# Kernel optimization log

Hardware: AMD Instinct MI355X
Metric: run time of the kernel (lower is better)

Reference implementation:

```python
import jax, jax.numpy as jnp
import numpy as np
import math

D_MODEL = 4096
N_HEADS = 32
D_HEAD = D_MODEL // N_HEADS
SEQ = 2048
BATCH = 1


def rope(x):
    # x: [B, H, S, D]; rotate pairs (even, odd) along last dim
    S = x.shape[2]
    D = x.shape[-1]
    theta = 1.0 / (10000.0 ** (jnp.arange(0, D, 2, dtype=jnp.float32) / D))  # [D/2]
    ang = jnp.arange(S, dtype=jnp.float32)[:, None] * theta[None, :]          # [S, D/2]
    cos = jnp.cos(ang)
    sin = jnp.sin(ang)
    x_even = x[..., ::2]
    x_odd = x[..., 1::2]
    rot_even = x_even * cos - x_odd * sin
    rot_odd = x_even * sin + x_odd * cos
    return jnp.stack((rot_even, rot_odd), axis=-1).reshape(x.shape)


def setup_inputs() -> dict:
    key = jax.random.key(0)
    ks = jax.random.split(key, 9)
    scale = 1.0 / math.sqrt(D_MODEL)
    return {
        "x": jax.random.normal(ks[0], (BATCH, SEQ, D_MODEL), dtype=jnp.float32),
        "Wq": jax.random.normal(ks[1], (D_MODEL, D_MODEL), dtype=jnp.float32) * scale,
        "bq": jnp.zeros((D_MODEL,), dtype=jnp.float32),
        "Wk": jax.random.normal(ks[2], (D_MODEL, D_MODEL), dtype=jnp.float32) * scale,
        "bk": jnp.zeros((D_MODEL,), dtype=jnp.float32),
        "Wv": jax.random.normal(ks[3], (D_MODEL, D_MODEL), dtype=jnp.float32) * scale,
        "bv": jnp.zeros((D_MODEL,), dtype=jnp.float32),
        "Wo": jax.random.normal(ks[4], (D_MODEL, D_MODEL), dtype=jnp.float32) * scale,
        "bo": jnp.zeros((D_MODEL,), dtype=jnp.float32),
    }


def reference(x, Wq, bq, Wk, bk, Wv, bv, Wo, bo):
    B, S, _ = x.shape
    def proj(W, b):
        h = x @ W.T + b  # torch Linear convention: y = x W^T + b
        return h.reshape(B, S, N_HEADS, D_HEAD).transpose(0, 2, 1, 3)  # [B,H,S,D]
    Q = rope(proj(Wq, bq))
    K = rope(proj(Wk, bk))
    V = proj(Wv, bv)
    scores = jnp.einsum('bhqd,bhkd->bhqk', Q, K) / math.sqrt(D_HEAD)
    causal = jnp.tril(jnp.ones((S, S), dtype=bool))
    scores = jnp.where(causal[None, None], scores, jnp.float32(-jnp.inf))
    attn = jax.nn.softmax(scores, axis=-1)
    out = jnp.einsum('bhqk,bhkd->bhqd', attn, V)
    out = out.transpose(0, 2, 1, 3).reshape(B, S, N_HEADS * D_HEAD)
    return out @ Wo.T + bo
```

## Files before the change

kernel.cpp:

```cpp
#include <hip/hip_runtime.h>
#include <hip/hip_bf16.h>

typedef __bf16 bf16x8 __attribute__((ext_vector_type(8)));
typedef float floatx4 __attribute__((ext_vector_type(4)));

__device__ __forceinline__ ushort f2bf(float f) {
  union { float f; unsigned u; } v; v.f = f;
  unsigned r = ((v.u >> 16) & 1u) + 0x7FFFu;
  return (ushort)((v.u + r) >> 16);
}
__device__ __forceinline__ float bf2f(ushort u) {
  union { unsigned u; float f; } v; v.u = ((unsigned)u) << 16;
  return v.f;
}

__device__ __forceinline__ void cp16(const void* g, void* l) {
  __builtin_amdgcn_global_load_lds((const __attribute__((address_space(1))) unsigned int*)g,
                                   (__attribute__((address_space(3))) unsigned int*)l,
                                   16, 0, 0);
}

__global__ __launch_bounds__(256) void cast_kernel(const float* __restrict__ in,
                                                   ushort* __restrict__ out) {
  size_t idx = (size_t)blockIdx.x * 256 + threadIdx.x;
  float4 v = ((const float4*)in)[idx];
  ushort4 o;
  o.x = f2bf(v.x); o.y = f2bf(v.y); o.z = f2bf(v.z); o.w = f2bf(v.w);
  ((ushort4*)out)[idx] = o;
}

template <int EPI>
__global__ __launch_bounds__(256) void gemm_bt(const ushort* __restrict__ A,
                                               const ushort* __restrict__ B,
                                               const float* __restrict__ bias,
                                               void* __restrict__ outp) {
  constexpr int K = 4096, N = 4096;
  __shared__ ushort As[2][128 * 32];
  __shared__ ushort Bs[2][128 * 32];

  unsigned bid = blockIdx.x;
  unsigned swz = (bid & 7u) * (gridDim.x >> 3) + (bid >> 3);
  int tm = swz >> 5;
  int tn = swz & 31;
  int m0 = tm << 7, n0 = tn << 7;

  int t = threadIdx.x;
  int l = t & 63;
  int w = t >> 6;
  int wm = (w >> 1) << 6;
  int wn = (w & 1) << 6;

  floatx4 zero4 = {0.f, 0.f, 0.f, 0.f};
  floatx4 acc[4][4];
#pragma unroll
  for (int i = 0; i < 4; ++i)
#pragma unroll
    for (int j = 0; j < 4; ++j) acc[i][j] = zero4;

  int rr = t >> 2;
  int sp = t & 3;

  auto stage = [&](int buf, int kt) {
    int k0 = kt << 5;
#pragma unroll
    for (int iss = 0; iss < 2; ++iss) {
      int r = iss * 64 + rr;
      int sl = sp ^ (r & 3);
      cp16(A + (size_t)(m0 + r) * K + k0 + sl * 8, &As[buf][(iss * 256 + t) * 8]);
      cp16(B + (size_t)(n0 + r) * K + k0 + sl * 8, &Bs[buf][(iss * 256 + t) * 8]);
    }
  };

  stage(0, 0);
  __syncthreads();
  int buf = 0;
  for (int kt = 0; kt < K / 32; ++kt) {
    if (kt + 1 < K / 32) stage(buf ^ 1, kt + 1);
    bf16x8 af[4], bfr[4];
#pragma unroll
    for (int i = 0; i < 4; ++i) {
      int ra = wm + i * 16 + (l & 15);
      af[i] = *(const bf16x8*)&As[buf][ra * 32 + (((l >> 4) ^ (ra & 3)) * 8)];
      int rb = wn + i * 16 + (l & 15);
      bfr[i] = *(const bf16x8*)&Bs[buf][rb * 32 + (((l >> 4) ^ (rb & 3)) * 8)];
    }
#pragma unroll
    for (int i = 0; i < 4; ++i)
#pragma unroll
      for (int j = 0; j < 4; ++j)
        acc[i][j] = __builtin_amdgcn_mfma_f32_16x16x32_bf16(af[i], bfr[j], acc[i][j], 0, 0, 0);
    __syncthreads();
    buf ^= 1;
  }

#pragma unroll
  for (int i = 0; i < 4; ++i)
#pragma unroll
    for (int j = 0; j < 4; ++j)
#pragma unroll
      for (int r = 0; r < 4; ++r) {
        int row = m0 + wm + i * 16 + ((l >> 4) << 2) + r;
        int col = n0 + wn + j * 16 + (l & 15);
        float v = acc[i][j][r] + bias[col];
        if constexpr (EPI == 0) {
          ((ushort*)outp)[((size_t)(col >> 7) * 2048 + row) * 128 + (col & 127)] = f2bf(v);
        } else {
          ((float*)outp)[(size_t)row * N + col] = v;
        }
      }
}

__global__ __launch_bounds__(256) void rope_kernel(ushort* __restrict__ Q,
                                                   ushort* __restrict__ K) {
  unsigned idx = blockIdx.x * 256 + threadIdx.x;
  ushort* p = blockIdx.y ? K : Q;
  int i4 = idx & 15;
  int s = (idx >> 4) & 2047;
  size_t base = ((size_t)(idx >> 15) * 2048 + s) * 128 + (size_t)i4 * 8;
  ushort v[8];
  *(uint4*)v = *(const uint4*)(p + base);
  const float C = 0.14391156516f;
#pragma unroll
  for (int j = 0; j < 4; ++j) {
    int i = i4 * 4 + j;
    float theta = expf(-C * (float)i);
    float ang = (float)s * theta;
    float cs = cosf(ang), sn = sinf(ang);
    float e = bf2f(v[2 * j]), o = bf2f(v[2 * j + 1]);
    v[2 * j]     = f2bf(e * cs - o * sn);
    v[2 * j + 1] = f2bf(e * sn + o * cs);
  }
  *(uint4*)(p + base) = *(uint4*)v;
}

__global__ __launch_bounds__(256) void transpose_v(const ushort* __restrict__ V,
                                                   ushort* __restrict__ Vt) {
  __shared__ ushort tile[64][72];
  int st = blockIdx.x, dt = blockIdx.y, h = blockIdx.z;
  int t = threadIdx.x;
  int rl = t >> 2, c16 = (t & 3) * 16;
  const ushort* src = V + ((size_t)(h * 2048 + st * 64 + rl)) * 128 + dt * 64 + c16;
  *(uint4*)&tile[rl][c16] = *(const uint4*)src;
  *(uint4*)&tile[rl][c16 + 8] = *(const uint4*)(src + 8);
  __syncthreads();
  int d = t >> 2, s16 = (t & 3) * 16;
  __align__(16) ushort tmp[16];
#pragma unroll
  for (int j = 0; j < 16; ++j) tmp[j] = tile[s16 + j][d];
  ushort* dst = Vt + ((size_t)(h * 128 + dt * 64 + d)) * 2048 + st * 64 + s16;
  *(uint4*)dst = *(uint4*)tmp;
  *(uint4*)(dst + 8) = *(uint4*)(tmp + 8);
}

__global__ __launch_bounds__(256) void attn_kernel(const ushort* __restrict__ Qb,
                                                   const ushort* __restrict__ Kb,
                                                   const ushort* __restrict__ Vt,
                                                   ushort* __restrict__ aO) {
  __shared__ ushort Ks[64 * 128];
  __shared__ ushort Vs[128 * 64];
  __shared__ ushort Ps[4][16 * 64];

  int qt = blockIdx.x;
  int h = blockIdx.y;
  int t = threadIdx.x;
  int l = t & 63;
  int w = t >> 6;

  bf16x8 qf[4];
  {
    int qrow = qt * 64 + w * 16 + (l & 15);
    const ushort* qp = Qb + ((size_t)(h * 2048 + qrow)) * 128 + ((l >> 4) * 8);
#pragma unroll
    for (int ks = 0; ks < 4; ++ks) qf[ks] = *(const bf16x8*)(qp + ks * 32);
  }

  float m[4], lsum[4];
#pragma unroll
  for (int r = 0; r < 4; ++r) { m[r] = -1e30f; lsum[r] = 0.f; }
  floatx4 zero4 = {0.f, 0.f, 0.f, 0.f};
  floatx4 oacc[8];
#pragma unroll
  for (int i = 0; i < 8; ++i) oacc[i] = zero4;

  const float scale = 0.08838834764831845f;

  for (int kt = 0; kt <= qt; ++kt) {
    {
      int rk = t >> 4, sk = t & 15;
      int rv = t >> 3, sv = t & 7;
#pragma unroll
      for (int iss = 0; iss < 4; ++iss) {
        int row = iss * 16 + rk;
        int sl = sk ^ (row & 7);
        cp16(Kb + ((size_t)(h * 2048 + kt * 64 + row)) * 128 + sl * 8,
             &Ks[(iss * 256 + t) * 8]);
        int rowv = iss * 32 + rv;
        int slv = sv ^ (rowv & 7);
        cp16(Vt + ((size_t)(h * 128 + rowv)) * 2048 + kt * 64 + slv * 8,
             &Vs[(iss * 256 + t) * 8]);
      }
    }
    __syncthreads();

    floatx4 sacc[4];
#pragma unroll
    for (int nt = 0; nt < 4; ++nt) sacc[nt] = zero4;
#pragma unroll
    for (int nt = 0; nt < 4; ++nt) {
      int row = nt * 16 + (l & 15);
#pragma unroll
      for (int ks = 0; ks < 4; ++ks) {
        bf16x8 kf = *(const bf16x8*)&Ks[row * 128 + (((ks * 4 + (l >> 4)) ^ (row & 7)) * 8)];
        sacc[nt] = __builtin_amdgcn_mfma_f32_16x16x32_bf16(qf[ks], kf, sacc[nt], 0, 0, 0);
      }
    }

    float sv_[4][4];
    float mt[4] = {-1e30f, -1e30f, -1e30f, -1e30f};
#pragma unroll
    for (int nt = 0; nt < 4; ++nt)
#pragma unroll
      for (int r = 0; r < 4; ++r) {
        float s = sacc[nt][r] * scale;
        if (kt == qt) {
          int kg = nt * 16 + (l & 15);
          int qg = w * 16 + ((l >> 4) << 2) + r;
          if (kg > qg) s = -1e30f;
        }
        sv_[nt][r] = s;
        mt[r] = fmaxf(mt[r], s);
      }
#pragma unroll
    for (int r = 0; r < 4; ++r)
#pragma unroll
      for (int msk = 1; msk < 16; msk <<= 1) mt[r] = fmaxf(mt[r], __shfl_xor(mt[r], msk, 64));

    float sf[4], mn[4];
#pragma unroll
    for (int r = 0; r < 4; ++r) {
      mn[r] = fmaxf(m[r], mt[r]);
      sf[r] = __expf(m[r] - mn[r]);
      m[r] = mn[r];
    }
#pragma unroll
    for (int i = 0; i < 8; ++i)
#pragma unroll
      for (int r = 0; r < 4; ++r) oacc[i][r] *= sf[r];

    float ps[4] = {0.f, 0.f, 0.f, 0.f};
    ushort* Pw = Ps[w];
#pragma unroll
    for (int nt = 0; nt < 4; ++nt)
#pragma unroll
      for (int r = 0; r < 4; ++r) {
        float p = __expf(sv_[nt][r] - mn[r]);
        ps[r] += p;
        int row = ((l >> 4) << 2) + r;
        int col = nt * 16 + (l & 15);
        int slot = (col >> 3) ^ (row & 7);
        Pw[row * 64 + slot * 8 + (col & 7)] = f2bf(p);
      }
#pragma unroll
    for (int r = 0; r < 4; ++r) {
#pragma unroll
      for (int msk = 1; msk < 16; msk <<= 1) ps[r] += __shfl_xor(ps[r], msk, 64);
      lsum[r] = lsum[r] * sf[r] + ps[r];
    }

    bf16x8 pf[2];
#pragma unroll
    for (int ks = 0; ks < 2; ++ks) {
      int row = l & 15;
      pf[ks] = *(const bf16x8*)&Pw[row * 64 + (((ks * 4 + (l >> 4)) ^ (row & 7)) * 8)];
    }
#pragma unroll
    for (int nt = 0; nt < 8; ++nt) {
      int row = nt * 16 + (l & 15);
#pragma unroll
      for (int ks = 0; ks < 2; ++ks) {
        bf16x8 vf = *(const bf16x8*)&Vs[row * 64 + (((ks * 4 + (l >> 4)) ^ (row & 7)) * 8)];
        oacc[nt] = __builtin_amdgcn_mfma_f32_16x16x32_bf16(pf[ks], vf, oacc[nt], 0, 0, 0);
      }
    }
    __syncthreads();
  }

  float inv[4];
#pragma unroll
  for (int r = 0; r < 4; ++r) inv[r] = 1.0f / lsum[r];
#pragma unroll
  for (int nt = 0; nt < 8; ++nt)
#pragma unroll
    for (int r = 0; r < 4; ++r) {
      int row = qt * 64 + w * 16 + ((l >> 4) << 2) + r;
      int col = h * 128 + nt * 16 + (l & 15);
      aO[(size_t)row * 4096 + col] = f2bf(oacc[nt][r] * inv[r]);
    }
}

extern "C" void kernel_launch(void* const* d_in, const int* in_sizes, int n_in,
                              void* d_out, int out_size, void* d_ws, size_t ws_size,
                              hipStream_t stream) {
  const float* x  = (const float*)d_in[0];
  const float* Wq = (const float*)d_in[1];
  const float* bq = (const float*)d_in[2];
  const float* Wk = (const float*)d_in[3];
  const float* bk = (const float*)d_in[4];
  const float* Wv = (const float*)d_in[5];
  const float* bv = (const float*)d_in[6];
  const float* Wo = (const float*)d_in[7];
  const float* bo = (const float*)d_in[8];
  float* out = (float*)d_out;

  char* ws = (char*)d_ws;
  ushort* Wb = (ushort*)(ws);
  ushort* xb = (ushort*)(ws + 33554432);
  ushort* Qb = (ushort*)(ws + 50331648);
  ushort* Kb = (ushort*)(ws + 67108864);
  ushort* Vb = (ushort*)(ws + 83886080);
  ushort* Vt = xb;
  ushort* aO = Vb;

  cast_kernel<<<8192, 256, 0, stream>>>(x, xb);
  cast_kernel<<<16384, 256, 0, stream>>>(Wq, Wb);
  gemm_bt<0><<<512, 256, 0, stream>>>(xb, Wb, bq, Qb);
  cast_kernel<<<16384, 256, 0, stream>>>(Wk, Wb);
  gemm_bt<0><<<512, 256, 0, stream>>>(xb, Wb, bk, Kb);
  cast_kernel<<<16384, 256, 0, stream>>>(Wv, Wb);
  gemm_bt<0><<<512, 256, 0, stream>>>(xb, Wb, bv, Vb);
  rope_kernel<<<dim3(4096, 2), 256, 0, stream>>>(Qb, Kb);
  transpose_v<<<dim3(32, 2, 32), 256, 0, stream>>>(Vb, Vt);
  attn_kernel<<<dim3(32, 32), 256, 0, stream>>>(Qb, Kb, Vt, aO);
  cast_kernel<<<16384, 256, 0, stream>>>(Wo, Wb);
  gemm_bt<1><<<512, 256, 0, stream>>>(aO, Wb, bo, out);
}
```

Baseline: 879.3 us.

## Rebalance causal attention with paired query tiles, double-buffered K/V, and RoPE table

The attention kernel now uses 512-thread blocks that each own a 128-row query tile pair (bi and 15-bi), so every block does the same number of causal key tiles. K/V staging into LDS is double-buffered so the next tile's loads overlap compute, and blocks are mapped so the heads sharing an XCD stay together. Warps whose rows are fully masked skip the tile. RoPE cos/sin values are precomputed once into a table in workspace instead of evaluating transcendentals per element. The cost is more LDS per block, fewer blocks (256), and an extra small kernel launch.

Result: faster. 793.1 us (-9.8%).

```diff
diff --git a/kernel.cpp b/kernel.cpp
--- a/kernel.cpp
+++ b/kernel.cpp
@@ -110,8 +110,19 @@
       }
 }
 
+__global__ __launch_bounds__(256) void rope_table(float2* __restrict__ tab) {
+  int idx = blockIdx.x * 256 + threadIdx.x;
+  int i = idx & 63;
+  int s = idx >> 6;
+  const float C = 0.14391156516f;
+  float theta = expf(-C * (float)i);
+  float ang = (float)s * theta;
+  tab[idx] = make_float2(cosf(ang), sinf(ang));
+}
+
 __global__ __launch_bounds__(256) void rope_kernel(ushort* __restrict__ Q,
-                                                   ushort* __restrict__ K) {
+                                                   ushort* __restrict__ K,
+                                                   const float2* __restrict__ tab) {
   unsigned idx = blockIdx.x * 256 + threadIdx.x;
   ushort* p = blockIdx.y ? K : Q;
   int i4 = idx & 15;
@@ -119,16 +130,12 @@
   size_t base = ((size_t)(idx >> 15) * 2048 + s) * 128 + (size_t)i4 * 8;
   ushort v[8];
   *(uint4*)v = *(const uint4*)(p + base);
-  const float C = 0.14391156516f;
 #pragma unroll
   for (int j = 0; j < 4; ++j) {
-    int i = i4 * 4 + j;
-    float theta = expf(-C * (float)i);
-    float ang = (float)s * theta;
-    float cs = cosf(ang), sn = sinf(ang);
+    float2 cs = tab[s * 64 + i4 * 4 + j];
     float e = bf2f(v[2 * j]), o = bf2f(v[2 * j + 1]);
-    v[2 * j]     = f2bf(e * cs - o * sn);
-    v[2 * j + 1] = f2bf(e * sn + o * cs);
+    v[2 * j]     = f2bf(e * cs.x - o * cs.y);
+    v[2 * j + 1] = f2bf(e * cs.y + o * cs.x);
   }
   *(uint4*)(p + base) = *(uint4*)v;
 }
@@ -152,150 +159,181 @@
   *(uint4*)(dst + 8) = *(uint4*)(tmp + 8);
 }
 
-__global__ __launch_bounds__(256) void attn_kernel(const ushort* __restrict__ Qb,
+__global__ __launch_bounds__(512) void attn_kernel(const ushort* __restrict__ Qb,
                                                    const ushort* __restrict__ Kb,
                                                    const ushort* __restrict__ Vt,
                                                    ushort* __restrict__ aO) {
-  __shared__ ushort Ks[64 * 128];
-  __shared__ ushort Vs[128 * 64];
-  __shared__ ushort Ps[4][16 * 64];
-
-  int qt = blockIdx.x;
-  int h = blockIdx.y;
+  __shared__ ushort Ks[2][64 * 128];
+  __shared__ ushort Vs[2][128 * 64];
+  __shared__ ushort Ps[8][16 * 64];
+
+  int bid = blockIdx.x;
+  int xcd = bid & 7, slot = bid >> 3;
+  int h = xcd * 4 + (slot >> 3);
+  int bi = slot & 7;
+
   int t = threadIdx.x;
   int l = t & 63;
   int w = t >> 6;
 
+  const int n0t = 2 * bi + 2;
+  const int NT = 34;
+
+  const float scale = 0.08838834764831845f;
+  floatx4 zero4 = {0.f, 0.f, 0.f, 0.f};
+
   bf16x8 qf[4];
-  {
-    int qrow = qt * 64 + w * 16 + (l & 15);
+  float m[4], lsum[4];
+  floatx4 oacc[8];
+
+  auto loadQ = [&](int qt) {
+    int qrow = qt * 128 + w * 16 + (l & 15);
     const ushort* qp = Qb + ((size_t)(h * 2048 + qrow)) * 128 + ((l >> 4) * 8);
 #pragma unroll
     for (int ks = 0; ks < 4; ++ks) qf[ks] = *(const bf16x8*)(qp + ks * 32);
+  };
+  auto resetState = [&]() {
+#pragma unroll
+    for (int r = 0; r < 4; ++r) { m[r] = -1e30f; lsum[r] = 0.f; }
+#pragma unroll
+    for (int i = 0; i < 8; ++i) oacc[i] = zero4;
+  };
+  auto flushO = [&](int qt) {
+    float inv[4];
+#pragma unroll
+    for (int r = 0; r < 4; ++r) inv[r] = 1.0f / lsum[r];
+#pragma unroll
+    for (int nt = 0; nt < 8; ++nt)
+#pragma unroll
+      for (int r = 0; r < 4; ++r) {
+        int row = qt * 128 + w * 16 + ((l >> 4) << 2) + r;
+        int col = h * 128 + nt * 16 + (l & 15);
+        aO[(size_t)row * 4096 + col] = f2bf(oacc[nt][r] * inv[r]);
+      }
+  };
+  auto stage = [&](int buf, int kt) {
+#pragma unroll
+    for (int iss = 0; iss < 2; ++iss) {
+      int uu = iss * 512 + t;
+      int rowk = uu >> 4, slk = (uu & 15) ^ (rowk & 7);
+      cp16(Kb + ((size_t)(h * 2048 + kt * 64 + rowk)) * 128 + slk * 8,
+           &Ks[buf][uu * 8]);
+      int rowv = uu >> 3, slv = (uu & 7) ^ (rowv & 7);
+      cp16(Vt + ((size_t)(h * 128 + rowv)) * 2048 + kt * 64 + slv * 8,
+           &Vs[buf][uu * 8]);
+    }
+  };
+
+  loadQ(bi);
+  resetState();
+  stage(0, 0);
+  __syncthreads();
+
+  int buf = 0;
+  for (int it = 0; it < NT; ++it) {
+    int qt = (it < n0t) ? bi : (15 - bi);
+    int kt = (it < n0t) ? it : (it - n0t);
+
+    if (it + 1 < NT) {
+      int kn = (it + 1 < n0t) ? (it + 1) : (it + 1 - n0t);
+      stage(buf ^ 1, kn);
+    }
+
+    if (it == n0t) {
+      flushO(bi);
+      resetState();
+      loadQ(15 - bi);
+    }
+
+    int q0 = qt * 128;
+    bool skipw = (kt * 64 > q0 + w * 16 + 15);
+    if (!skipw) {
+      floatx4 sacc[4];
+#pragma unroll
+      for (int nt = 0; nt < 4; ++nt) sacc[nt] = zero4;
+#pragma unroll
+      for (int nt = 0; nt < 4; ++nt) {
+        int row = nt * 16 + (l & 15);
+#pragma unroll
+        for (int ks = 0; ks < 4; ++ks) {
+          bf16x8 kf = *(const bf16x8*)&Ks[buf][row * 128 + (((ks * 4 + (l >> 4)) ^ (row & 7)) * 8)];
+          sacc[nt] = __builtin_amdgcn_mfma_f32_16x16x32_bf16(qf[ks], kf, sacc[nt], 0, 0, 0);
+        }
+      }
+
+      bool diag = (kt * 64 + 63 > q0 + w * 16);
+      float sv_[4][4];
+      float mt[4] = {-1e30f, -1e30f, -1e30f, -1e30f};
+#pragma unroll
+      for (int nt = 0; nt < 4; ++nt)
+#pragma unroll
+        for (int r = 0; r < 4; ++r) {
+          float s = sacc[nt][r] * scale;
+          if (diag) {
+            int kg = kt * 64 + nt * 16 + (l & 15);
+            int qg = q0 + w * 16 + ((l >> 4) << 2) + r;
+            if (kg > qg) s = -1e30f;
+          }
+          sv_[nt][r] = s;
+          mt[r] = fmaxf(mt[r], s);
+        }
+#pragma unroll
+      for (int r = 0; r < 4; ++r)
+#pragma unroll
+        for (int msk = 1; msk < 16; msk <<= 1) mt[r] = fmaxf(mt[r], __shfl_xor(mt[r], msk, 64));
+
+      float sf[4], mn[4];
+#pragma unroll
+      for (int r = 0; r < 4; ++r) {
+        mn[r] = fmaxf(m[r], mt[r]);
+        sf[r] = __expf(m[r] - mn[r]);
+        m[r] = mn[r];
+      }
+#pragma unroll
+      for (int i = 0; i < 8; ++i)
+#pragma unroll
+        for (int r = 0; r < 4; ++r) oacc[i][r] *= sf[r];
+
+      float ps[4] = {0.f, 0.f, 0.f, 0.f};
+      ushort* Pw = Ps[w];
+#pragma unroll
+      for (int nt = 0; nt < 4; ++nt)
+#pragma unroll
+        for (int r = 0; r < 4; ++r) {
+          float p = __expf(sv_[nt][r] - mn[r]);
+          ps[r] += p;
+          int row = ((l >> 4) << 2) + r;
+          int col = nt * 16 + (l & 15);
+          int sl = (col >> 3) ^ (row & 7);
+          Pw[row * 64 + sl * 8 + (col & 7)] = f2bf(p);
+        }
+#pragma unroll
+      for (int r = 0; r < 4; ++r) {
+#pragma unroll
+        for (int msk = 1; msk < 16; msk <<= 1) ps[r] += __shfl_xor(ps[r], msk, 64);
+        lsum[r] = lsum[r] * sf[r] + ps[r];
+      }
+
+      bf16x8 pf[2];
+#pragma unroll
+      for (int ks = 0; ks < 2; ++ks) {
+        int row = l & 15;
+        pf[ks] = *(const bf16x8*)&Pw[row * 64 + (((ks * 4 + (l >> 4)) ^ (row & 7)) * 8)];
+      }
+#pragma unroll
+      for (int nt = 0; nt < 8; ++nt) {
+        int row = nt * 16 + (l & 15);
+#pragma unroll
+        for (int ks = 0; ks < 2; ++ks) {
+          bf16x8 vf = *(const bf16x8*)&Vs[buf][row * 64 + (((ks * 4 + (l >> 4)) ^ (row & 7)) * 8)];
+          oacc[nt] = __builtin_amdgcn_mfma_f32_16x16x32_bf16(pf[ks], vf, oacc[nt], 0, 0, 0);
+        }
+      }
+    }
+    __syncthreads();
+    buf ^= 1;
   }
-
-  float m[4], lsum[4];
-#pragma unroll
-  for (int r = 0; r < 4; ++r) { m[r] = -1e30f; lsum[r] = 0.f; }
-  floatx4 zero4 = {0.f, 0.f, 0.f, 0.f};
-  floatx4 oacc[8];
-#pragma unroll
-  for (int i = 0; i < 8; ++i) oacc[i] = zero4;
-
-  const float scale = 0.08838834764831845f;
-
-  for (int kt = 0; kt <= qt; ++kt) {
-    {
-      int rk = t >> 4, sk = t & 15;
-      int rv = t >> 3, sv = t & 7;
-#pragma unroll
-      for (int iss = 0; iss < 4; ++iss) {
-        int row = iss * 16 + rk;
-        int sl = sk ^ (row & 7);
-        cp16(Kb + ((size_t)(h * 2048 + kt * 64 + row)) * 128 + sl * 8,
-             &Ks[(iss * 256 + t) * 8]);
-        int rowv = iss * 32 + rv;
-        int slv = sv ^ (rowv & 7);
-        cp16(Vt + ((size_t)(h * 128 + rowv)) * 2048 + kt * 64 + slv * 8,
-             &Vs[(iss * 256 + t) * 8]);
-      }
-    }
-    __syncthreads();
-
-    floatx4 sacc[4];
-#pragma unroll
-    for (int nt = 0; nt < 4; ++nt) sacc[nt] = zero4;
-#pragma unroll
-    for (int nt = 0; nt < 4; ++nt) {
-      int row = nt * 16 + (l & 15);
-#pragma unroll
-      for (int ks = 0; ks < 4; ++ks) {
-        bf16x8 kf = *(const bf16x8*)&Ks[row * 128 + (((ks * 4 + (l >> 4)) ^ (row & 7)) * 8)];
-        sacc[nt] = __builtin_amdgcn_mfma_f32_16x16x32_bf16(qf[ks], kf, sacc[nt], 0, 0, 0);
-      }
-    }
-
-    float sv_[4][4];
-    float mt[4] = {-1e30f, -1e30f, -1e30f, -1e30f};
-#pragma unroll
-    for (int nt = 0; nt < 4; ++nt)
-#pragma unroll
-      for (int r = 0; r < 4; ++r) {
-        float s = sacc[nt][r] * scale;
-        if (kt == qt) {
-          int kg = nt * 16 + (l & 15);
-          int qg = w * 16 + ((l >> 4) << 2) + r;
-          if (kg > qg) s = -1e30f;
-        }
-        sv_[nt][r] = s;
-        mt[r] = fmaxf(mt[r], s);
-      }
-#pragma unroll
-    for (int r = 0; r < 4; ++r)
-#pragma unroll
-      for (int msk = 1; msk < 16; msk <<= 1) mt[r] = fmaxf(mt[r], __shfl_xor(mt[r], msk, 64));
-
-    float sf[4], mn[4];
-#pragma unroll
-    for (int r = 0; r < 4; ++r) {
-      mn[r] = fmaxf(m[r], mt[r]);
-      sf[r] = __expf(m[r] - mn[r]);
-      m[r] = mn[r];
-    }
-#pragma unroll
-    for (int i = 0; i < 8; ++i)
-#pragma unroll
-      for (int r = 0; r < 4; ++r) oacc[i][r] *= sf[r];
-
-    float ps[4] = {0.f, 0.f, 0.f, 0.f};
-    ushort* Pw = Ps[w];
-#pragma unroll
-    for (int nt = 0; nt < 4; ++nt)
-#pragma unroll
-      for (int r = 0; r < 4; ++r) {
-        float p = __expf(sv_[nt][r] - mn[r]);
-        ps[r] += p;
-        int row = ((l >> 4) << 2) + r;
-        int col = nt * 16 + (l & 15);
-        int slot = (col >> 3) ^ (row & 7);
-        Pw[row * 64 + slot * 8 + (col & 7)] = f2bf(p);
-      }
-#pragma unroll
-    for (int r = 0; r < 4; ++r) {
-#pragma unroll
-      for (int msk = 1; msk < 16; msk <<= 1) ps[r] += __shfl_xor(ps[r], msk, 64);
-      lsum[r] = lsum[r] * sf[r] + ps[r];
-    }
-
-    bf16x8 pf[2];
-#pragma unroll
-    for (int ks = 0; ks < 2; ++ks) {
-      int row = l & 15;
-      pf[ks] = *(const bf16x8*)&Pw[row * 64 + (((ks * 4 + (l >> 4)) ^ (row & 7)) * 8)];
-    }
-#pragma unroll
-    for (int nt = 0; nt < 8; ++nt) {
-      int row = nt * 16 + (l & 15);
-#pragma unroll
-      for (int ks = 0; ks < 2; ++ks) {
-        bf16x8 vf = *(const bf16x8*)&Vs[row * 64 + (((ks * 4 + (l >> 4)) ^ (row & 7)) * 8)];
-        oacc[nt] = __builtin_amdgcn_mfma_f32_16x16x32_bf16(pf[ks], vf, oacc[nt], 0, 0, 0);
-      }
-    }
-    __syncthreads();
-  }
-
-  float inv[4];
-#pragma unroll
-  for (int r = 0; r < 4; ++r) inv[r] = 1.0f / lsum[r];
-#pragma unroll
-  for (int nt = 0; nt < 8; ++nt)
-#pragma unroll
-    for (int r = 0; r < 4; ++r) {
-      int row = qt * 64 + w * 16 + ((l >> 4) << 2) + r;
-      int col = h * 128 + nt * 16 + (l & 15);
-      aO[(size_t)row * 4096 + col] = f2bf(oacc[nt][r] * inv[r]);
-    }
+  flushO(15 - bi);
 }
 
 extern "C" void kernel_launch(void* const* d_in, const int* in_sizes, int n_in,
@@ -320,6 +358,7 @@
   ushort* Vb = (ushort*)(ws + 83886080);
   ushort* Vt = xb;
   ushort* aO = Vb;
+  float2* tab = (float2*)Wb;
 
   cast_kernel<<<8192, 256, 0, stream>>>(x, xb);
   cast_kernel<<<16384, 256, 0, stream>>>(Wq, Wb);
@@ -328,9 +367,10 @@
   gemm_bt<0><<<512, 256, 0, stream>>>(xb, Wb, bk, Kb);
   cast_kernel<<<16384, 256, 0, stream>>>(Wv, Wb);
   gemm_bt<0><<<512, 256, 0, stream>>>(xb, Wb, bv, Vb);
-  rope_kernel<<<dim3(4096, 2), 256, 0, stream>>>(Qb, Kb);
+  rope_table<<<512, 256, 0, stream>>>(tab);
+  rope_kernel<<<dim3(4096, 2), 256, 0, stream>>>(Qb, Kb, tab);
   transpose_v<<<dim3(32, 2, 32), 256, 0, stream>>>(Vb, Vt);
-  attn_kernel<<<dim3(32, 32), 256, 0, stream>>>(Qb, Kb, Vt, aO);
+  attn_kernel<<<256, 512, 0, stream>>>(Qb, Kb, Vt, aO);
   cast_kernel<<<16384, 256, 0, stream>>>(Wo, Wb);
   gemm_bt<1><<<512, 256, 0, stream>>>(aO, Wb, bo, out);
 }
```
